# Kernel optimization log

Measured on AMD Instinct MI355X. Metric: run time of the kernel, lower is better.

The kernel has to match this reference:

```python
import jax, jax.numpy as jnp
import numpy as np

BITS = 4
MAXQ = 15           # 2**BITS - 1
PACK = 32 // BITS   # 8 nibbles per int32
GROUP = 128         # quantization group size along in_features


def _unpack_rows(packed, rows):
    """Unpack int32-packed 4-bit values along axis 0. packed: [Kp, N] -> [rows, N]."""
    shifts = jnp.arange(0, 32, BITS, dtype=jnp.int32)            # [PACK]
    u = (packed[:, None, :] >> shifts[None, :, None]) & MAXQ    # [Kp, PACK, N]
    return u.reshape(-1, packed.shape[1])[:rows]


def _unpack_cols(packed, cols):
    """Unpack int32-packed 4-bit values along axis 1. packed: [G, Np] -> [G, cols]."""
    shifts = jnp.arange(0, 32, BITS, dtype=jnp.int32)            # [PACK]
    u = (packed[:, :, None] >> shifts[None, None, :]) & MAXQ    # [G, Np, PACK]
    return u.reshape(packed.shape[0], -1)[:, :cols]


def setup_inputs() -> dict:
    key = jax.random.key(0)
    k1, k2, k3, k4, k5 = jax.random.split(key, 5)
    K, N = 4096, 11008
    x = jax.random.normal(k1, (4, 2048, K), dtype=jnp.float32)
    qweight = jax.random.randint(k2, (K // PACK, N), 0, 2**31 - 1, dtype=jnp.int32)
    scales = jax.random.uniform(k3, (K // GROUP, N), dtype=jnp.float32)
    qzeros = jax.random.randint(k4, (K // GROUP, (N + PACK - 1) // PACK), 0, 2**31 - 1, dtype=jnp.int32)
    bias = jax.random.normal(k5, (N,), dtype=jnp.float32)
    return {"x": x, "qweight": qweight, "scales": scales, "qzeros": qzeros, "bias": bias}


def reference(x, qweight, scales, qzeros, bias):
    K = x.shape[-1]
    N = scales.shape[1]
    qw = _unpack_rows(qweight, K)            # [K, N] int in [0, 15]
    qz = _unpack_cols(qzeros, N) + 1         # [G, N] int in [1, 16] (+1 per get_unpacked_params)
    s = jnp.repeat(scales, GROUP, axis=0)    # [K, N]  groupwise -> per-row
    z = jnp.repeat(qz, GROUP, axis=0)        # [K, N]
    W = (qw - z).astype(x.dtype) * s         # dequantized weight [K, N]
    out = jnp.matmul(x, W) + bias
    return out.astype(x.dtype)
```

## Files before the change

### kernel.cpp

```cpp
#include <hip/hip_runtime.h>
#include <hip/hip_bf16.h>
#include <stdint.h>

typedef __attribute__((ext_vector_type(4))) float f32x4;
typedef __attribute__((ext_vector_type(8))) short bf16x8;
typedef __attribute__((ext_vector_type(8))) unsigned short ushort8;
typedef __attribute__((ext_vector_type(4))) unsigned short ushort4v;

__device__ __forceinline__ unsigned short f2bf(float f) {
    union { float f; unsigned int u; } v; v.f = f;
    unsigned int u = v.u;
    u += 0x7FFFu + ((u >> 16) & 1u);
    return (unsigned short)(u >> 16);
}

__device__ __forceinline__ int swz(int row, int k) {
    return (row * 64 + k) ^ ((row & 7) << 3);
}

__device__ __forceinline__ void gld16(const void* g, void* l) {
    __builtin_amdgcn_global_load_lds(
        (const __attribute__((address_space(1))) unsigned int*)g,
        (__attribute__((address_space(3))) unsigned int*)l,
        16, 0, 0);
}

__global__ __launch_bounds__(256)
void prep(const float* __restrict__ X, const int* __restrict__ QW,
          const float* __restrict__ SC, const int* __restrict__ QZ,
          unsigned short* __restrict__ Xb, unsigned short* __restrict__ WT,
          int N, int K, long long n8, int deqB) {
    const int bid = blockIdx.x;
    const int t = threadIdx.x;
    if (bid < deqB) {
        const int ntiles = N >> 6;
        const int nb = bid % ntiles;
        const int kb = bid / ntiles;
        const int n0 = nb * 64, kp0 = kb * 64;
        #pragma unroll
        for (int w = 0; w < 16; ++w) {
            const int p = t + 256 * w;
            const int kpo = p & 63, ni = p >> 6;
            const int n = n0 + ni, kp = kp0 + kpo;
            const int g = kp >> 4;
            const float s = SC[(size_t)g * N + n];
            const int zq = ((QZ[(size_t)g * (N >> 3) + (n >> 3)] >> ((n & 7) * 4)) & 15) + 1;
            const float zb = -(float)zq * s;
            const unsigned int q = (unsigned int)QW[(size_t)kp * N + n];
            ushort8 o;
            #pragma unroll
            for (int j = 0; j < 8; ++j)
                o[j] = f2bf(fmaf((float)((q >> (4 * j)) & 15u), s, zb));
            *reinterpret_cast<ushort8*>(&WT[(size_t)n * K + kp * 8]) = o;
        }
    } else {
        long long i0 = (long long)(bid - deqB) * 256 + t;
        long long stride = (long long)(gridDim.x - deqB) * 256;
        for (long long i = i0; i < n8; i += stride) {
            const float4* p = reinterpret_cast<const float4*>(X + i * 8);
            float4 a = p[0], b = p[1];
            ushort8 o;
            o[0] = f2bf(a.x); o[1] = f2bf(a.y); o[2] = f2bf(a.z); o[3] = f2bf(a.w);
            o[4] = f2bf(b.x); o[5] = f2bf(b.y); o[6] = f2bf(b.z); o[7] = f2bf(b.w);
            *reinterpret_cast<ushort8*>(Xb + i * 8) = o;
        }
    }
}

__global__ __launch_bounds__(256)
void cvt_x(const float* __restrict__ X, unsigned short* __restrict__ Xb, long long n8) {
    long long i0 = (long long)blockIdx.x * 256 + threadIdx.x;
    long long stride = (long long)gridDim.x * 256;
    for (long long i = i0; i < n8; i += stride) {
        const float4* p = reinterpret_cast<const float4*>(X + i * 8);
        float4 a = p[0], b = p[1];
        ushort8 o;
        o[0] = f2bf(a.x); o[1] = f2bf(a.y); o[2] = f2bf(a.z); o[3] = f2bf(a.w);
        o[4] = f2bf(b.x); o[5] = f2bf(b.y); o[6] = f2bf(b.z); o[7] = f2bf(b.w);
        *reinterpret_cast<ushort8*>(Xb + i * 8) = o;
    }
}

__global__ __launch_bounds__(256)
void deq_w(const int* __restrict__ QW, const float* __restrict__ SC,
           const int* __restrict__ QZ, unsigned short* __restrict__ WT,
           int N, int K) {
    const int ntiles = N >> 6;
    const int nb = blockIdx.x % ntiles;
    const int kb = blockIdx.x / ntiles;
    const int n0 = nb * 64, kp0 = kb * 64;
    const int t = threadIdx.x;
    #pragma unroll
    for (int w = 0; w < 16; ++w) {
        const int p = t + 256 * w;
        const int kpo = p & 63, ni = p >> 6;
        const int n = n0 + ni, kp = kp0 + kpo;
        const int g = kp >> 4;
        const float s = SC[(size_t)g * N + n];
        const int zq = ((QZ[(size_t)g * (N >> 3) + (n >> 3)] >> ((n & 7) * 4)) & 15) + 1;
        const float zb = -(float)zq * s;
        const unsigned int q = (unsigned int)QW[(size_t)kp * N + n];
        ushort8 o;
        #pragma unroll
        for (int j = 0; j < 8; ++j)
            o[j] = f2bf(fmaf((float)((q >> (4 * j)) & 15u), s, zb));
        *reinterpret_cast<ushort8*>(&WT[(size_t)n * K + kp * 8]) = o;
    }
}

template<int KC, int NC, int NTN>
__global__ __launch_bounds__(512, 2)
void qgemm_256(const unsigned short* __restrict__ Xb, const unsigned short* __restrict__ WT,
               const float* __restrict__ BIAS, float* __restrict__ OUT, int M) {
    __shared__ __align__(16) unsigned short S[65536];

    int id = blockIdx.x;
    const int nwg = gridDim.x;
    if ((nwg & 7) == 0) id = (id & 7) * (nwg >> 3) + (id >> 3);

    const int bm = (id / NTN) << 8;
    const int bn = (id % NTN) << 8;
    const int tid = threadIdx.x;
    const int lane = tid & 63;
    const int wid = tid >> 6;
    const int wm = (wid >> 2) * 64;
    const int wn = (wid & 3) * 32;
    const int lr = lane & 15;
    const int lk = (lane >> 4) * 8;

    const int xr  = (lr & 7) << 3;
    const int lo0 = lk ^ xr;
    const int lo1 = (32 + lk) ^ xr;
    const int lrow = lr * 64;

    f32x4 acc[8][4] = {};
    constexpr int nk = KC >> 6;

    const int srow = tid >> 3;
    const int scol = ((tid & 7) ^ (srow & 7)) << 3;
    const unsigned short* gA[2] = { Xb + (size_t)(bm + srow) * KC + scol,
                                    Xb + (size_t)(bm + 128 + srow) * KC + scol };
    const unsigned short* gB[2] = { WT + (size_t)(bn + srow) * KC + scol,
                                    WT + (size_t)(bn + 128 + srow) * KC + scol };

    auto stage = [&](int buf, int tt, int kind, int half) {
        const unsigned short* g = (kind ? gB[half] : gA[half]) + (size_t)tt * 64;
        unsigned short* lb = S + (kind ? 32768 : 0) + buf * 16384 + half * 8192 + tid * 8;
        gld16(g, lb);
        gld16(g + (size_t)64 * KC, lb + 4096);
    };

    bf16x8 aL[4][2], aH[4][2], bL[2][2], bH[2][2];

    auto loadA = [&](bf16x8 (&dst)[4][2], const unsigned short* Sa, int rbase) {
        const unsigned short* p = Sa + rbase * 64 + lrow;
        #pragma unroll
        for (int i = 0; i < 4; ++i) {
            dst[i][0] = *reinterpret_cast<const bf16x8*>(p + i * 1024 + lo0);
            dst[i][1] = *reinterpret_cast<const bf16x8*>(p + i * 1024 + lo1);
        }
    };
    auto loadB = [&](bf16x8 (&dst)[2][2], const unsigned short* Sb, int rbase) {
        const unsigned short* p = Sb + rbase * 64 + lrow;
        #pragma unroll
        for (int j = 0; j < 2; ++j) {
            dst[j][0] = *reinterpret_cast<const bf16x8*>(p + j * 1024 + lo0);
            dst[j][1] = *reinterpret_cast<const bf16x8*>(p + j * 1024 + lo1);
        }
    };
    auto quad = [&](bf16x8 (&A)[4][2], bf16x8 (&B)[2][2], int mi0, int nj0) {
        __builtin_amdgcn_s_setprio(1);
        #pragma unroll
        for (int kk = 0; kk < 2; ++kk)
            #pragma unroll
            for (int i = 0; i < 4; ++i)
                #pragma unroll
                for (int j = 0; j < 2; ++j)
                    acc[mi0 + i][nj0 + j] = __builtin_amdgcn_mfma_f32_16x16x32_bf16(
                        A[i][kk], B[j][kk], acc[mi0 + i][nj0 + j], 0, 0, 0);
        __builtin_amdgcn_s_setprio(0);
    };

    stage(0, 0, 0, 0); stage(0, 0, 0, 1);
    stage(0, 0, 1, 0); stage(0, 0, 1, 1);
    stage(1, 1, 0, 0); stage(1, 1, 1, 1); stage(1, 1, 0, 1);
    asm volatile("s_waitcnt vmcnt(6)" ::: "memory");

    for (int t = 0; t < nk; ++t) {
        const int c = t & 1;
        const unsigned short* Sa = S + c * 16384;
        const unsigned short* Sb = S + 32768 + c * 16384;

        if (t + 1 < nk) stage(c ^ 1, t + 1, 1, 0);

        __builtin_amdgcn_s_barrier();
        loadA(aL, Sa, wm);
        loadB(bL, Sb, wn);
        loadB(bH, Sb, 128 + wn);
        quad(aL, bL, 0, 0);
        __builtin_amdgcn_s_barrier();

        if (t + 2 < nk) stage(c, t + 2, 0, 0);
        quad(aL, bH, 0, 2);
        loadA(aH, Sa, 128 + wm);
        __builtin_amdgcn_s_barrier();

        if (t + 2 < nk) stage(c, t + 2, 1, 1);
        quad(aH, bL, 4, 0);
        __builtin_amdgcn_s_barrier();

        if (t + 2 < nk) {
            stage(c, t + 2, 0, 1);
            quad(aH, bH, 4, 2);
            asm volatile("s_waitcnt vmcnt(6)" ::: "memory");
        } else {
            quad(aH, bH, 4, 2);
            asm volatile("s_waitcnt vmcnt(0)" ::: "memory");
        }
    }

    #pragma unroll
    for (int mi = 0; mi < 8; ++mi) {
        const int row = bm + wm + (mi & 3) * 16 + ((mi >> 2) ? 128 : 0) + (lane >> 4) * 4;
        #pragma unroll
        for (int nj = 0; nj < 4; ++nj) {
            const int col = bn + wn + (nj & 1) * 16 + ((nj >> 1) ? 128 : 0) + lr;
            const float b = BIAS[col];
            #pragma unroll
            for (int r = 0; r < 4; ++r)
                OUT[(size_t)(row + r) * NC + col] = acc[mi][nj][r] + b;
        }
    }
}

__global__ __launch_bounds__(256, 2)
void qgemm_ws(const unsigned short* __restrict__ Xb, const unsigned short* __restrict__ WT,
              const float* __restrict__ BIAS, float* __restrict__ OUT,
              int M, int N, int K, int n0, int ntn) {
    __shared__ __align__(16) unsigned short As[2][128 * 64];
    __shared__ __align__(16) unsigned short Bs[2][128 * 64];

    const int bm = (blockIdx.x / ntn) * 128;
    const int bn = n0 + (blockIdx.x % ntn) * 128;
    const int tid = threadIdx.x;
    const int lane = tid & 63;
    const int wave = tid >> 6;
    const int wm = (wave >> 1) * 64, wn = (wave & 1) * 64;
    const int lr = lane & 15, lk = (lane >> 4) * 8;

    f32x4 acc[4][4] = {};
    const int nk = K >> 6;

    auto stage = [&](int buf, int t) {
        const int k0 = t * 64;
        #pragma unroll
        for (int p = 0; p < 4; ++p) {
            const int slot = p * 256 + tid;
            const int row = slot >> 3, c = slot & 7;
            const int gk = k0 + ((c ^ (row & 7)) << 3);
            gld16(Xb + (size_t)(bm + row) * K + gk, &As[buf][slot * 8]);
            gld16(WT + (size_t)(bn + row) * K + gk, &Bs[buf][slot * 8]);
        }
    };

    auto compute = [&](int buf) {
        #pragma unroll
        for (int kk = 0; kk < 2; ++kk) {
            bf16x8 af[4], bfr[4];
            #pragma unroll
            for (int i = 0; i < 4; ++i) {
                af[i]  = *reinterpret_cast<const bf16x8*>(&As[buf][swz(wm + i * 16 + lr, kk * 32 + lk)]);
                bfr[i] = *reinterpret_cast<const bf16x8*>(&Bs[buf][swz(wn + i * 16 + lr, kk * 32 + lk)]);
            }
            #pragma unroll
            for (int i = 0; i < 4; ++i)
                #pragma unroll
                for (int j = 0; j < 4; ++j)
                    acc[i][j] = __builtin_amdgcn_mfma_f32_16x16x32_bf16(af[i], bfr[j], acc[i][j], 0, 0, 0);
        }
    };

    stage(0, 0);
    __syncthreads();
    int cur = 0;
    for (int t = 0; t < nk; ++t) {
        if (t + 1 < nk) stage(cur ^ 1, t + 1);
        compute(cur);
        __syncthreads();
        cur ^= 1;
    }

    #pragma unroll
    for (int i = 0; i < 4; ++i) {
        #pragma unroll
        for (int j = 0; j < 4; ++j) {
            const int col = bn + wn + j * 16 + lr;
            const float b = BIAS[col];
            #pragma unroll
            for (int r = 0; r < 4; ++r) {
                const int row = bm + wm + i * 16 + (lane >> 4) * 4 + r;
                OUT[(size_t)row * N + col] = acc[i][j][r] + b;
            }
        }
    }
}

__global__ __launch_bounds__(256, 2)
void qgemm_fb(const float* __restrict__ X, const int* __restrict__ QW,
              const float* __restrict__ SC, const int* __restrict__ QZ,
              const float* __restrict__ BIAS, float* __restrict__ OUT,
              int M, int N, int K) {
    __shared__ __align__(16) unsigned short As[2][128 * 64];
    __shared__ __align__(16) unsigned short Bs[2][128 * 64];

    const int ntn = N / 128;
    const int bm = (blockIdx.x / ntn) * 128;
    const int bn = (blockIdx.x % ntn) * 128;
    const int tid  = threadIdx.x;
    const int lane = tid & 63;
    const int wave = tid >> 6;
    const int wm = (wave >> 1) * 64, wn = (wave & 1) * 64;
    const int lr = lane & 15, lk = (lane >> 4) * 8;
    const int a_c4 = tid & 15, a_r0 = tid >> 4;
    const int b_n  = tid & 127, b_k0 = tid >> 7;

    f32x4 acc[4][4] = {};
    float4 va[8];
    unsigned int wb[4];
    float sc_s = 0.f, sc_zb = 0.f;
    const int nk = K / 64;

    auto gload = [&](int t) {
        const int k0 = t * 64;
        #pragma unroll
        for (int p = 0; p < 8; ++p)
            va[p] = *reinterpret_cast<const float4*>(X + (size_t)(bm + a_r0 + p * 16) * K + k0 + a_c4 * 4);
        const int g  = k0 >> 7;
        const int gn = bn + b_n;
        sc_s = SC[(size_t)g * N + gn];
        const int zq = ((QZ[(size_t)g * (N >> 3) + (gn >> 3)] >> ((gn & 7) * 4)) & 15) + 1;
        sc_zb = -(float)zq * sc_s;
        #pragma unroll
        for (int p = 0; p < 4; ++p)
            wb[p] = (unsigned int)QW[(size_t)(t * 8 + b_k0 + p * 2) * N + gn];
    };

    auto lwrite = [&](int buf) {
        #pragma unroll
        for (int p = 0; p < 8; ++p) {
            const int row = a_r0 + p * 16;
            ushort4v b;
            b.x = f2bf(va[p].x); b.y = f2bf(va[p].y);
            b.z = f2bf(va[p].z); b.w = f2bf(va[p].w);
            *reinterpret_cast<ushort4v*>(&As[buf][swz(row, a_c4 * 4)]) = b;
        }
        #pragma unroll
        for (int p = 0; p < 4; ++p) {
            const int ko = b_k0 + p * 2;
            ushort8 o;
            #pragma unroll
            for (int j = 0; j < 8; ++j)
                o[j] = f2bf(fmaf((float)((wb[p] >> (4 * j)) & 15u), sc_s, sc_zb));
            *reinterpret_cast<ushort8*>(&Bs[buf][swz(b_n, ko * 8)]) = o;
        }
    };

    auto compute = [&](int buf) {
        #pragma unroll
        for (int kk = 0; kk < 2; ++kk) {
            bf16x8 af[4], bfr[4];
            #pragma unroll
            for (int i = 0; i < 4; ++i) {
                af[i]  = *reinterpret_cast<const bf16x8*>(&As[buf][swz(wm + i * 16 + lr, kk * 32 + lk)]);
                bfr[i] = *reinterpret_cast<const bf16x8*>(&Bs[buf][swz(wn + i * 16 + lr, kk * 32 + lk)]);
            }
            #pragma unroll
            for (int i = 0; i < 4; ++i)
                #pragma unroll
                for (int j = 0; j < 4; ++j)
                    acc[i][j] = __builtin_amdgcn_mfma_f32_16x16x32_bf16(af[i], bfr[j], acc[i][j], 0, 0, 0);
        }
    };

    gload(0); lwrite(0);
    __syncthreads();
    for (int t = 0; t < nk; ++t) {
        if (t + 1 < nk) gload(t + 1);
        compute(t & 1);
        if (t + 1 < nk) lwrite((t + 1) & 1);
        __syncthreads();
    }

    #pragma unroll
    for (int i = 0; i < 4; ++i) {
        #pragma unroll
        for (int j = 0; j < 4; ++j) {
            const int col = bn + wn + j * 16 + lr;
            const float b = BIAS[col];
            #pragma unroll
            for (int r = 0; r < 4; ++r) {
                const int row = bm + wm + i * 16 + (lane >> 4) * 4 + r;
                OUT[(size_t)row * N + col] = acc[i][j][r] + b;
            }
        }
    }
}

extern "C" void kernel_launch(void* const* d_in, const int* in_sizes, int n_in,
                              void* d_out, int out_size, void* d_ws, size_t ws_size,
                              hipStream_t stream) {
    const float* X    = (const float*)d_in[0];
    const int*   QW   = (const int*)d_in[1];
    const float* SC   = (const float*)d_in[2];
    const int*   QZ   = (const int*)d_in[3];
    const float* BIAS = (const float*)d_in[4];
    float* OUT = (float*)d_out;

    const int N = in_sizes[4];
    const long long qwsz = in_sizes[1];
    const int K = (int)(qwsz * 8 / N);
    const int M = in_sizes[0] / K;

    const size_t xb_bytes = (size_t)M * K * 2;
    const size_t wt_bytes = (size_t)N * K * 2;

    if (ws_size >= xb_bytes + wt_bytes) {
        unsigned short* Xb = (unsigned short*)d_ws;
        unsigned short* WT = Xb + (size_t)M * K;

        if (K == 4096 && N == 11008 && (M % 256) == 0) {
            const int deqB = (N >> 6) * (K / 512);
            prep<<<deqB + 2048, 256, 0, stream>>>(X, QW, SC, QZ, Xb, WT,
                                                  N, K, (long long)M * K / 8, deqB);
            qgemm_256<4096, 11008, 40><<<(M / 256) * 40, 512, 0, stream>>>(Xb, WT, BIAS, OUT, M);
            qgemm_ws<<<(M / 128) * 6, 256, 0, stream>>>(Xb, WT, BIAS, OUT, M, N, K, 10240, 6);
        } else {
            cvt_x<<<2048, 256, 0, stream>>>(X, Xb, (long long)M * K / 8);
            deq_w<<<(N >> 6) * (K / 512), 256, 0, stream>>>(QW, SC, QZ, WT, N, K);
            qgemm_ws<<<(M / 128) * (N / 128), 256, 0, stream>>>(Xb, WT, BIAS, OUT, M, N, K, 0, N / 128);
        }
    } else {
        qgemm_fb<<<(M / 128) * (N / 128), 256, 0, stream>>>(X, QW, SC, QZ, BIAS, OUT, M, N, K);
    }
}
```

Baseline: 763.3 us.

## Merge 256-tile GEMM and tail GEMM into one mixed-tile kernel launch

Replaces the separate 256x256 main GEMM launch and the 128x128 tail GEMM launch (covering the last 768 columns) with a single kernel. Block IDs below the big-tile count run the existing 256x256 path, and the rest run a new 512-thread 128x128 tail path with double-buffered LDS. This is meant to remove the serialized tail launch and let tail blocks fill idle CUs while the big tiles finish. The tail path now uses a simpler synchronous pipeline at 512 threads, and its blocks are scheduled after all the big tiles.

```diff
diff --git a/kernel.cpp b/kernel.cpp
--- a/kernel.cpp
+++ b/kernel.cpp
@@ -108,127 +108,195 @@
     }
 }
 
-template<int KC, int NC, int NTN>
+template<int KC, int NC, int NTN, int TC>
 __global__ __launch_bounds__(512, 2)
-void qgemm_256(const unsigned short* __restrict__ Xb, const unsigned short* __restrict__ WT,
+void qgemm_mix(const unsigned short* __restrict__ Xb, const unsigned short* __restrict__ WT,
                const float* __restrict__ BIAS, float* __restrict__ OUT, int M) {
     __shared__ __align__(16) unsigned short S[65536];
 
-    int id = blockIdx.x;
-    const int nwg = gridDim.x;
-    if ((nwg & 7) == 0) id = (id & 7) * (nwg >> 3) + (id >> 3);
-
-    const int bm = (id / NTN) << 8;
-    const int bn = (id % NTN) << 8;
     const int tid = threadIdx.x;
     const int lane = tid & 63;
     const int wid = tid >> 6;
-    const int wm = (wid >> 2) * 64;
-    const int wn = (wid & 3) * 32;
     const int lr = lane & 15;
     const int lk = (lane >> 4) * 8;
-
-    const int xr  = (lr & 7) << 3;
-    const int lo0 = lk ^ xr;
-    const int lo1 = (32 + lk) ^ xr;
-    const int lrow = lr * 64;
-
-    f32x4 acc[8][4] = {};
     constexpr int nk = KC >> 6;
 
-    const int srow = tid >> 3;
-    const int scol = ((tid & 7) ^ (srow & 7)) << 3;
-    const unsigned short* gA[2] = { Xb + (size_t)(bm + srow) * KC + scol,
-                                    Xb + (size_t)(bm + 128 + srow) * KC + scol };
-    const unsigned short* gB[2] = { WT + (size_t)(bn + srow) * KC + scol,
-                                    WT + (size_t)(bn + 128 + srow) * KC + scol };
-
-    auto stage = [&](int buf, int tt, int kind, int half) {
-        const unsigned short* g = (kind ? gB[half] : gA[half]) + (size_t)tt * 64;
-        unsigned short* lb = S + (kind ? 32768 : 0) + buf * 16384 + half * 8192 + tid * 8;
-        gld16(g, lb);
-        gld16(g + (size_t)64 * KC, lb + 4096);
-    };
-
-    bf16x8 aL[4][2], aH[4][2], bL[2][2], bH[2][2];
-
-    auto loadA = [&](bf16x8 (&dst)[4][2], const unsigned short* Sa, int rbase) {
-        const unsigned short* p = Sa + rbase * 64 + lrow;
+    const int bid0 = blockIdx.x;
+    const int BIG = (M >> 8) * NTN;
+
+    if (bid0 < BIG) {
+        int id = bid0;
+        if ((BIG & 7) == 0) id = (id & 7) * (BIG >> 3) + (id >> 3);
+
+        const int bm = (id / NTN) << 8;
+        const int bn = (id % NTN) << 8;
+        const int wm = (wid >> 2) * 64;
+        const int wn = (wid & 3) * 32;
+
+        const int xr  = (lr & 7) << 3;
+        const int lo0 = lk ^ xr;
+        const int lo1 = (32 + lk) ^ xr;
+        const int lrow = lr * 64;
+
+        f32x4 acc[8][4] = {};
+
+        const int srow = tid >> 3;
+        const int scol = ((tid & 7) ^ (srow & 7)) << 3;
+        const unsigned short* gA[2] = { Xb + (size_t)(bm + srow) * KC + scol,
+                                        Xb + (size_t)(bm + 128 + srow) * KC + scol };
+        const unsigned short* gB[2] = { WT + (size_t)(bn + srow) * KC + scol,
+                                        WT + (size_t)(bn + 128 + srow) * KC + scol };
+
+        auto stage = [&](int buf, int tt, int kind, int half) {
+            const unsigned short* g = (kind ? gB[half] : gA[half]) + (size_t)tt * 64;
+            unsigned short* lb = S + (kind ? 32768 : 0) + buf * 16384 + half * 8192 + tid * 8;
+            gld16(g, lb);
+            gld16(g + (size_t)64 * KC, lb + 4096);
+        };
+
+        bf16x8 aL[4][2], aH[4][2], bL[2][2], bH[2][2];
+
+        auto loadA = [&](bf16x8 (&dst)[4][2], const unsigned short* Sa, int rbase) {
+            const unsigned short* p = Sa + rbase * 64 + lrow;
+            #pragma unroll
+            for (int i = 0; i < 4; ++i) {
+                dst[i][0] = *reinterpret_cast<const bf16x8*>(p + i * 1024 + lo0);
+                dst[i][1] = *reinterpret_cast<const bf16x8*>(p + i * 1024 + lo1);
+            }
+        };
+        auto loadB = [&](bf16x8 (&dst)[2][2], const unsigned short* Sb, int rbase) {
+            const unsigned short* p = Sb + rbase * 64 + lrow;
+            #pragma unroll
+            for (int j = 0; j < 2; ++j) {
+                dst[j][0] = *reinterpret_cast<const bf16x8*>(p + j * 1024 + lo0);
+                dst[j][1] = *reinterpret_cast<const bf16x8*>(p + j * 1024 + lo1);
+            }
+        };
+        auto quad = [&](bf16x8 (&A)[4][2], bf16x8 (&B)[2][2], int mi0, int nj0) {
+            __builtin_amdgcn_s_setprio(1);
+            #pragma unroll
+            for (int kk = 0; kk < 2; ++kk)
+                #pragma unroll
+                for (int i = 0; i < 4; ++i)
+                    #pragma unroll
+                    for (int j = 0; j < 2; ++j)
+                        acc[mi0 + i][nj0 + j] = __builtin_amdgcn_mfma_f32_16x16x32_bf16(
+                            A[i][kk], B[j][kk], acc[mi0 + i][nj0 + j], 0, 0, 0);
+            __builtin_amdgcn_s_setprio(0);
+        };
+
+        stage(0, 0, 0, 0); stage(0, 0, 0, 1);
+        stage(0, 0, 1, 0); stage(0, 0, 1, 1);
+        stage(1, 1, 0, 0); stage(1, 1, 1, 1); stage(1, 1, 0, 1);
+        asm volatile("s_waitcnt vmcnt(6)" ::: "memory");
+
+        for (int t = 0; t < nk; ++t) {
+            const int c = t & 1;
+            const unsigned short* Sa = S + c * 16384;
+            const unsigned short* Sb = S + 32768 + c * 16384;
+
+            if (t + 1 < nk) stage(c ^ 1, t + 1, 1, 0);
+
+            __builtin_amdgcn_s_barrier();
+            loadA(aL, Sa, wm);
+            loadB(bL, Sb, wn);
+            loadB(bH, Sb, 128 + wn);
+            quad(aL, bL, 0, 0);
+            __builtin_amdgcn_s_barrier();
+
+            if (t + 2 < nk) stage(c, t + 2, 0, 0);
+            quad(aL, bH, 0, 2);
+            loadA(aH, Sa, 128 + wm);
+            __builtin_amdgcn_s_barrier();
+
+            if (t + 2 < nk) stage(c, t + 2, 1, 1);
+            quad(aH, bL, 4, 0);
+            __builtin_amdgcn_s_barrier();
+
+            if (t + 2 < nk) {
+                stage(c, t + 2, 0, 1);
+                quad(aH, bH, 4, 2);
+                asm volatile("s_waitcnt vmcnt(6)" ::: "memory");
+            } else {
+                quad(aH, bH, 4, 2);
+                asm volatile("s_waitcnt vmcnt(0)" ::: "memory");
+            }
+        }
+
+        #pragma unroll
+        for (int mi = 0; mi < 8; ++mi) {
+            const int row = bm + wm + (mi & 3) * 16 + ((mi >> 2) ? 128 : 0) + (lane >> 4) * 4;
+            #pragma unroll
+            for (int nj = 0; nj < 4; ++nj) {
+                const int col = bn + wn + (nj & 1) * 16 + ((nj >> 1) ? 128 : 0) + lr;
+                const float b = BIAS[col];
+                #pragma unroll
+                for (int r = 0; r < 4; ++r)
+                    OUT[(size_t)(row + r) * NC + col] = acc[mi][nj][r] + b;
+            }
+        }
+    } else {
+        const int id2 = bid0 - BIG;
+        const int bm = (id2 / TC) * 128;
+        const int bn = NTN * 256 + (id2 % TC) * 128;
+        const int wm2 = (wid >> 2) * 64;
+        const int wn2 = (wid & 3) * 32;
+
+        f32x4 acc2[4][2] = {};
+
+        auto stg = [&](int buf, int t) {
+            unsigned short* la = S + buf * 8192;
+            unsigned short* lb2 = S + 16384 + buf * 8192;
+            #pragma unroll
+            for (int p = 0; p < 2; ++p) {
+                const int slot = p * 512 + tid;
+                const int row = slot >> 3, c = slot & 7;
+                const int gk = t * 64 + ((c ^ (row & 7)) << 3);
+                gld16(Xb + (size_t)(bm + row) * KC + gk, la + slot * 8);
+                gld16(WT + (size_t)(bn + row) * KC + gk, lb2 + slot * 8);
+            }
+        };
+        auto cmp = [&](int buf) {
+            const unsigned short* la = S + buf * 8192;
+            const unsigned short* lb2 = S + 16384 + buf * 8192;
+            #pragma unroll
+            for (int kk = 0; kk < 2; ++kk) {
+                bf16x8 af[4], bfr[2];
+                #pragma unroll
+                for (int i = 0; i < 4; ++i)
+                    af[i] = *reinterpret_cast<const bf16x8*>(&la[swz(wm2 + i * 16 + lr, kk * 32 + lk)]);
+                #pragma unroll
+                for (int j = 0; j < 2; ++j)
+                    bfr[j] = *reinterpret_cast<const bf16x8*>(&lb2[swz(wn2 + j * 16 + lr, kk * 32 + lk)]);
+                #pragma unroll
+                for (int i = 0; i < 4; ++i)
+                    #pragma unroll
+                    for (int j = 0; j < 2; ++j)
+                        acc2[i][j] = __builtin_amdgcn_mfma_f32_16x16x32_bf16(
+                            af[i], bfr[j], acc2[i][j], 0, 0, 0);
+            }
+        };
+
+        stg(0, 0);
+        __syncthreads();
+        for (int t = 0; t < nk; ++t) {
+            if (t + 1 < nk) stg((t + 1) & 1, t + 1);
+            cmp(t & 1);
+            __syncthreads();
+        }
+
         #pragma unroll
         for (int i = 0; i < 4; ++i) {
-            dst[i][0] = *reinterpret_cast<const bf16x8*>(p + i * 1024 + lo0);
-            dst[i][1] = *reinterpret_cast<const bf16x8*>(p + i * 1024 + lo1);
-        }
-    };
-    auto loadB = [&](bf16x8 (&dst)[2][2], const unsigned short* Sb, int rbase) {
-        const unsigned short* p = Sb + rbase * 64 + lrow;
-        #pragma unroll
-        for (int j = 0; j < 2; ++j) {
-            dst[j][0] = *reinterpret_cast<const bf16x8*>(p + j * 1024 + lo0);
-            dst[j][1] = *reinterpret_cast<const bf16x8*>(p + j * 1024 + lo1);
-        }
-    };
-    auto quad = [&](bf16x8 (&A)[4][2], bf16x8 (&B)[2][2], int mi0, int nj0) {
-        __builtin_amdgcn_s_setprio(1);
-        #pragma unroll
-        for (int kk = 0; kk < 2; ++kk)
-            #pragma unroll
-            for (int i = 0; i < 4; ++i)
-                #pragma unroll
-                for (int j = 0; j < 2; ++j)
-                    acc[mi0 + i][nj0 + j] = __builtin_amdgcn_mfma_f32_16x16x32_bf16(
-                        A[i][kk], B[j][kk], acc[mi0 + i][nj0 + j], 0, 0, 0);
-        __builtin_amdgcn_s_setprio(0);
-    };
-
-    stage(0, 0, 0, 0); stage(0, 0, 0, 1);
-    stage(0, 0, 1, 0); stage(0, 0, 1, 1);
-    stage(1, 1, 0, 0); stage(1, 1, 1, 1); stage(1, 1, 0, 1);
-    asm volatile("s_waitcnt vmcnt(6)" ::: "memory");
-
-    for (int t = 0; t < nk; ++t) {
-        const int c = t & 1;
-        const unsigned short* Sa = S + c * 16384;
-        const unsigned short* Sb = S + 32768 + c * 16384;
-
-        if (t + 1 < nk) stage(c ^ 1, t + 1, 1, 0);
-
-        __builtin_amdgcn_s_barrier();
-        loadA(aL, Sa, wm);
-        loadB(bL, Sb, wn);
-        loadB(bH, Sb, 128 + wn);
-        quad(aL, bL, 0, 0);
-        __builtin_amdgcn_s_barrier();
-
-        if (t + 2 < nk) stage(c, t + 2, 0, 0);
-        quad(aL, bH, 0, 2);
-        loadA(aH, Sa, 128 + wm);
-        __builtin_amdgcn_s_barrier();
-
-        if (t + 2 < nk) stage(c, t + 2, 1, 1);
-        quad(aH, bL, 4, 0);
-        __builtin_amdgcn_s_barrier();
-
-        if (t + 2 < nk) {
-            stage(c, t + 2, 0, 1);
-            quad(aH, bH, 4, 2);
-            asm volatile("s_waitcnt vmcnt(6)" ::: "memory");
-        } else {
-            quad(aH, bH, 4, 2);
-            asm volatile("s_waitcnt vmcnt(0)" ::: "memory");
-        }
-    }
-
-    #pragma unroll
-    for (int mi = 0; mi < 8; ++mi) {
-        const int row = bm + wm + (mi & 3) * 16 + ((mi >> 2) ? 128 : 0) + (lane >> 4) * 4;
-        #pragma unroll
-        for (int nj = 0; nj < 4; ++nj) {
-            const int col = bn + wn + (nj & 1) * 16 + ((nj >> 1) ? 128 : 0) + lr;
-            const float b = BIAS[col];
-            #pragma unroll
-            for (int r = 0; r < 4; ++r)
-                OUT[(size_t)(row + r) * NC + col] = acc[mi][nj][r] + b;
+            #pragma unroll
+            for (int j = 0; j < 2; ++j) {
+                const int col = bn + wn2 + j * 16 + lr;
+                const float b = BIAS[col];
+                #pragma unroll
+                for (int r = 0; r < 4; ++r) {
+                    const int row = bm + wm2 + i * 16 + (lane >> 4) * 4 + r;
+                    OUT[(size_t)row * NC + col] = acc2[i][j][r] + b;
+                }
+            }
         }
     }
 }
@@ -432,8 +500,9 @@
             const int deqB = (N >> 6) * (K / 512);
             prep<<<deqB + 2048, 256, 0, stream>>>(X, QW, SC, QZ, Xb, WT,
                                                   N, K, (long long)M * K / 8, deqB);
-            qgemm_256<4096, 11008, 40><<<(M / 256) * 40, 512, 0, stream>>>(Xb, WT, BIAS, OUT, M);
-            qgemm_ws<<<(M / 128) * 6, 256, 0, stream>>>(Xb, WT, BIAS, OUT, M, N, K, 10240, 6);
+            const int big  = (M / 256) * 40;
+            const int tail = (M / 128) * 6;
+            qgemm_mix<4096, 11008, 40, 6><<<big + tail, 512, 0, stream>>>(Xb, WT, BIAS, OUT, M);
         } else {
             cvt_x<<<2048, 256, 0, stream>>>(X, Xb, (long long)M * K / 8);
             deq_w<<<(N >> 6) * (K / 512), 256, 0, stream>>>(QW, SC, QZ, WT, N, K);
```

Result: no change. 749.2 us (-1.8%).
